# Optimization experiments

Measured on AMD Instinct MI355X. Metric: run time of the kernel, lower is better.

The kernel has to match this reference:

```python
import jax, jax.numpy as jnp
import numpy as np

N_NODES = 50000
N_EDGES = 800000
NFEAT, NHID, NCLASS = 512, 128, 16


def _with_self_loops(edge_idx, n):
    loop = jnp.arange(n, dtype=edge_idx.dtype)
    src = jnp.concatenate([edge_idx[0], loop])  # [E+N]
    dst = jnp.concatenate([edge_idx[1], loop])
    return src, dst


def gcn_conv(x, src, dst, W, b, n):
    # GCNConv with add aggregation, self-loops, symmetric normalization.
    h = x @ W  # [N, out]
    ones = jnp.ones(src.shape[0], dtype=h.dtype)
    deg = jax.ops.segment_sum(ones, dst, num_segments=n)  # in-degree incl. self-loops
    dinv = jnp.where(deg > 0, jax.lax.rsqrt(deg), 0.0)
    norm = dinv[src] * dinv[dst]  # [E+N]
    msg = h[src] * norm[:, None]  # gather + scale
    out = jax.ops.segment_sum(msg, dst, num_segments=n)  # scatter-add
    return out + b


def setup_inputs() -> dict:
    key = jax.random.key(0)
    ks = jax.random.split(key, 8)
    x = jax.random.normal(ks[0], (N_NODES, NFEAT), dtype=jnp.float32)
    edge_idx = jax.random.randint(ks[1], (2, N_EDGES), 0, N_NODES, dtype=jnp.int64)
    s1 = 1.0 / np.sqrt(NFEAT)
    s2 = 1.0 / np.sqrt(NHID)
    W1 = jax.random.uniform(ks[2], (NFEAT, NHID), jnp.float32, -s1, s1)
    b1 = jnp.zeros((NHID,), jnp.float32)
    W2 = jax.random.uniform(ks[3], (NHID, NHID), jnp.float32, -s2, s2)
    b2 = jnp.zeros((NHID,), jnp.float32)
    Wc = jax.random.uniform(ks[4], (NHID, NCLASS), jnp.float32, -s2, s2)
    bc = jax.random.uniform(ks[5], (NCLASS,), jnp.float32, -s2, s2)
    return {"x": x, "edge_idx": edge_idx, "W1": W1, "b1": b1, "W2": W2, "b2": b2, "Wc": Wc, "bc": bc}


def reference(x, edge_idx, W1, b1, W2, b2, Wc, bc):
    n = x.shape[0]
    src, dst = _with_self_loops(edge_idx, n)
    h = gcn_conv(x, src, dst, W1, b1, n)
    h = jax.nn.relu(h)  # dropout is identity in eval mode
    h = gcn_conv(h, src, dst, W2, b2, n)
    h = jax.nn.relu(h)
    logits = h @ Wc + bc
    return jax.nn.log_softmax(logits, axis=1)
```

## Files before the change

### kernel.cpp

```cpp
#include <hip/hip_runtime.h>
#include <math.h>

#define NFEAT 512
#define NHID  128
#define NCLASS 16
#define SCAN_BS 512
#define AGG_BLOCKS 1024
#define NSTREAMS 16384

typedef __attribute__((ext_vector_type(8))) short short8;
typedef __attribute__((ext_vector_type(4))) float f32x4;

static __device__ __forceinline__ ushort f2b(float f) {
    union { float f; uint u; } v; v.f = f;
    uint r = v.u + 0x7FFFu + ((v.u >> 16) & 1u);
    return (ushort)(r >> 16);
}
static __device__ __forceinline__ float b2f_lo(uint bits) {
    union { uint u; float f; } v; v.u = bits << 16; return v.f;
}
static __device__ __forceinline__ float b2f_hi(uint bits) {
    union { uint u; float f; } v; v.u = bits & 0xffff0000u; return v.f;
}


__global__ void k_init_tcast(const float* __restrict__ W1, const float* __restrict__ W2,
                             ushort* __restrict__ W1T, ushort* __restrict__ W2T,
                             int* __restrict__ deg, int n) {
    int idx = blockIdx.x * 256 + threadIdx.x;
    if (idx < n) deg[idx] = 1;
    if (idx < NFEAT * 128) {
        int k = idx >> 7, c = idx & 127;
        W1T[(size_t)c * NFEAT + k] = f2b(W1[idx]);
    } else {
        int j = idx - NFEAT * 128;
        if (j < NHID * 128) {
            int k = j >> 7, c = j & 127;
            W2T[(size_t)c * NHID + k] = f2b(W2[j]);
        }
    }
}

__global__ void k_count(const int* __restrict__ dst, int e, int* __restrict__ deg,
                        int* __restrict__ ticket) {
    int i = blockIdx.x * blockDim.x + threadIdx.x;
    if (i < e) ticket[i] = atomicAdd(&deg[dst[i]], 1);
}

__global__ void k_scan1(const int* __restrict__ deg, float* __restrict__ dinv,
                        int* __restrict__ offs, int* __restrict__ bsum, int n) {
    __shared__ int s[SCAN_BS];
    int t = threadIdx.x;
    int i = blockIdx.x * SCAN_BS + t;
    int d = (i < n) ? deg[i] : 0;
    if (i < n) dinv[i] = rsqrtf((float)d);
    s[t] = d;
    for (int off = 1; off < SCAN_BS; off <<= 1) {
        __syncthreads();
        int x = (t >= off) ? s[t - off] : 0;
        __syncthreads();
        s[t] += x;
    }
    __syncthreads();
    if (i < n) offs[i] = s[t] - d;
    if (t == SCAN_BS - 1) bsum[blockIdx.x] = s[t];
}

__global__ void k_scan3(int* __restrict__ offs, const int* __restrict__ bsum, int nb, int n) {
    __shared__ int pref[128];
    int t = threadIdx.x;
    if (t < 64) {
        int carry = 0;
        for (int base = 0; base < nb; base += 64) {
            int j = base + t;
            int v = (j < nb) ? bsum[j] : 0;
            for (int off = 1; off < 64; off <<= 1) {
                int x = __shfl_up(v, off);
                if (t >= off) v += x;
            }
            if (j < nb) pref[j] = carry + v;
            carry += __shfl(v, 63);
        }
    }
    __syncthreads();
    int i = blockIdx.x * SCAN_BS + t;
    int add = blockIdx.x ? pref[blockIdx.x - 1] : 0;
    if (i < n) offs[i] += add;
    if (blockIdx.x == 0 && t == 0) offs[n] = pref[nb - 1];
}

__global__ void k_fill_edges(const int* __restrict__ src, const int* __restrict__ dst, int e,
                             const int* __restrict__ eoffs, const int* __restrict__ ticket,
                             uint* __restrict__ colp32, int* __restrict__ rankgs,
                             int n, int S) {
    int i = blockIdx.x * blockDim.x + threadIdx.x;
    if (i < e) {
        colp32[eoffs[dst[i]] + ticket[i] - 1] = (uint)src[i];
    }
    if (i < n) {
        colp32[eoffs[i + 1] - 1] = (uint)i | ((uint)(i + 1) << 16);
    }
    if (i < NSTREAMS) {
        int len = (S + NSTREAMS - 1) / NSTREAMS;
        int target = i * len;
        int lo = 0, hi = n;
        while (lo < hi) {
            int mid = (lo + hi) >> 1;
            if (eoffs[mid] < target) lo = mid + 1; else hi = mid;
        }
        rankgs[i] = eoffs[lo];
        if (i == 0) rankgs[NSTREAMS] = S;
    }
    if (i == 0) {
#pragma unroll
        for (int k = 0; k < 8; k++) colp32[S + k] = 0;
    }
}


template<int A_F32>
__global__ __launch_bounds__(256) void k_gemm(const void* __restrict__ Aptr,
                                              const ushort* __restrict__ WT,
                                              const float* __restrict__ rowscale,
                                              ushort* __restrict__ Hs, int M, int K) {
    __shared__ ushort As[64][40];
    __shared__ ushort Bs[128][40];

    const int tid = threadIdx.x;
    const int wc = tid >> 6, lane = tid & 63;
    const int lr = lane & 15, lk = (lane >> 4) * 8;
    const int rowbase = blockIdx.x * 64;

    f32x4 acc[4][2];
#pragma unroll
    for (int i = 0; i < 4; i++)
#pragma unroll
        for (int j = 0; j < 2; j++) acc[i][j] = (f32x4)0.f;

    const int sr = tid >> 2;
    const int sh = (tid & 3) * 8;

    for (int k0 = 0; k0 < K; k0 += 32) {
        {
            int gr = rowbase + sr;
            ushort tmp[8];
            if (A_F32) {
                const float* A = (const float*)Aptr;
                if (gr < M) {
                    const float* p = A + (size_t)gr * K + k0 + sh;
#pragma unroll
                    for (int q = 0; q < 2; q++) {
                        float4 v = *(const float4*)(p + q * 4);
                        tmp[q * 4 + 0] = f2b(v.x); tmp[q * 4 + 1] = f2b(v.y);
                        tmp[q * 4 + 2] = f2b(v.z); tmp[q * 4 + 3] = f2b(v.w);
                    }
                } else {
#pragma unroll
                    for (int q = 0; q < 8; q++) tmp[q] = 0;
                }
            } else {
                const ushort* A = (const ushort*)Aptr;
                if (gr < M) {
                    *(short8*)&tmp[0] = *(const short8*)(A + (size_t)gr * K + k0 + sh);
                } else {
#pragma unroll
                    for (int q = 0; q < 8; q++) tmp[q] = 0;
                }
            }
            *(short8*)&As[sr][sh] = *(short8*)&tmp[0];
        }
        {
#pragma unroll
            for (int t = 0; t < 2; t++) {
                int c = tid + t * 256;
                int row = c >> 2, q = c & 3;
                short8 v = *(const short8*)(WT + (size_t)row * K + k0 + q * 8);
                *(short8*)&Bs[row][q * 8] = v;
            }
        }
        __syncthreads();

        short8 af[4], bfv[2];
#pragma unroll
        for (int i = 0; i < 4; i++) af[i] = *(const short8*)&As[i * 16 + lr][lk];
#pragma unroll
        for (int j = 0; j < 2; j++) bfv[j] = *(const short8*)&Bs[wc * 32 + j * 16 + lr][lk];
#pragma unroll
        for (int i = 0; i < 4; i++)
#pragma unroll
            for (int j = 0; j < 2; j++)
                acc[i][j] = __builtin_amdgcn_mfma_f32_16x16x32_bf16(af[i], bfv[j], acc[i][j], 0, 0, 0);
        __syncthreads();
    }

#pragma unroll
    for (int i = 0; i < 4; i++) {
#pragma unroll
        for (int r = 0; r < 4; r++) {
            int row = rowbase + i * 16 + (lane >> 4) * 4 + r;
            if (row < M) {
                float sc = rowscale[row];
#pragma unroll
                for (int j = 0; j < 2; j++) {
                    int f = j * 16 + lr;
                    Hs[((size_t)wc * M + row) * 32 + f] = f2b(acc[i][j][r] * sc);
                }
            }
        }
    }
}


__global__ __launch_bounds__(256) void k_aggs(const ushort* __restrict__ hs,
                                              const uint* __restrict__ colp32,
                                              const int* __restrict__ rankgs,
                                              const float* __restrict__ dinv,
                                              const float* __restrict__ bias,
                                              ushort* __restrict__ outp, int n) {
    const int b = blockIdx.x;
    const int s = b & 3;
    const int wid = threadIdx.x >> 6, lane = threadIdx.x & 63;
    const int st16 = lane >> 2, q = lane & 3;
    const int stream = (((b >> 2) << 2) + wid) * 16 + st16;
    int gs = rankgs[stream];
    int se = rankgs[stream + 1];
    bool alive = gs < se;
    int g = gs;

    const ushort* hsl = hs + (size_t)s * n * 32;
    const float4 bv0 = *(const float4*)(bias + s * 32 + q * 8);
    const float4 bv1 = *(const float4*)(bias + s * 32 + q * 8 + 4);

    const uint* cp = colp32 + g;
    uint cw0 = cp[0], cw1 = cp[1], cw2 = cp[2], cw3 = cp[3];
    uint4 pk0 = *(const uint4*)(hsl + (size_t)(cw0 & 0xffffu) * 32 + q * 8);
    uint4 pk1 = *(const uint4*)(hsl + (size_t)(cw1 & 0xffffu) * 32 + q * 8);
    uint4 pk2 = *(const uint4*)(hsl + (size_t)(cw2 & 0xffffu) * 32 + q * 8);
    float fdv0 = (cw0 >> 16) ? dinv[(cw0 >> 16) - 1] : 0.f;
    float fdv1 = (cw1 >> 16) ? dinv[(cw1 >> 16) - 1] : 0.f;
    float fdv2 = (cw2 >> 16) ? dinv[(cw2 >> 16) - 1] : 0.f;
    float a0 = 0.f, a1 = 0.f, a2 = 0.f, a3 = 0.f;
    float a4 = 0.f, a5 = 0.f, a6 = 0.f, a7 = 0.f;

    while (__any(alive)) {
        if (alive) {
            uint cw4 = cp[4];
            uint4 pk3 = *(const uint4*)(hsl + (size_t)(cw3 & 0xffffu) * 32 + q * 8);
            float fdv3 = (cw3 >> 16) ? dinv[(cw3 >> 16) - 1] : 0.f;

            a0 += b2f_lo(pk0.x); a1 += b2f_hi(pk0.x);
            a2 += b2f_lo(pk0.y); a3 += b2f_hi(pk0.y);
            a4 += b2f_lo(pk0.z); a5 += b2f_hi(pk0.z);
            a6 += b2f_lo(pk0.w); a7 += b2f_hi(pk0.w);

            if (cw0 >> 16) {
                int v = (int)(cw0 >> 16) - 1;
                float r0 = fmaxf(fmaf(a0, fdv0, bv0.x), 0.f);
                float r1 = fmaxf(fmaf(a1, fdv0, bv0.y), 0.f);
                float r2 = fmaxf(fmaf(a2, fdv0, bv0.z), 0.f);
                float r3 = fmaxf(fmaf(a3, fdv0, bv0.w), 0.f);
                float r4 = fmaxf(fmaf(a4, fdv0, bv1.x), 0.f);
                float r5 = fmaxf(fmaf(a5, fdv0, bv1.y), 0.f);
                float r6 = fmaxf(fmaf(a6, fdv0, bv1.z), 0.f);
                float r7 = fmaxf(fmaf(a7, fdv0, bv1.w), 0.f);
                uint4 u;
                u.x = (uint)f2b(r0) | ((uint)f2b(r1) << 16);
                u.y = (uint)f2b(r2) | ((uint)f2b(r3) << 16);
                u.z = (uint)f2b(r4) | ((uint)f2b(r5) << 16);
                u.w = (uint)f2b(r6) | ((uint)f2b(r7) << 16);
                *(uint4*)(outp + (size_t)v * 128 + s * 32 + q * 8) = u;
                a0 = a1 = a2 = a3 = a4 = a5 = a6 = a7 = 0.f;
                if (g + 1 >= se) alive = false;
            }
            g++; cp++;
            cw0 = cw1; cw1 = cw2; cw2 = cw3; cw3 = cw4;
            pk0 = pk1; pk1 = pk2; pk2 = pk3;
            fdv0 = fdv1; fdv1 = fdv2; fdv2 = fdv3;
        }
    }
}


__global__ __launch_bounds__(256) void k_classify(const ushort* __restrict__ h,
                                                  const float* __restrict__ Wc,
                                                  const float* __restrict__ bc,
                                                  float* __restrict__ out, int n) {
    __shared__ float Ws[128 * 16];
    int tid = threadIdx.x;
#pragma unroll
    for (int t = 0; t < 8; t++) Ws[tid + 256 * t] = Wc[tid + 256 * t];
    __syncthreads();

    int wid = tid >> 6, lane = tid & 63;
    int v = blockIdx.x * 4 + wid;
    if (v >= n) return;

    int j = lane & 15, c = lane >> 4;
    const ushort* hv = h + (size_t)v * 128 + c * 32;
    float acc = 0.f;
#pragma unroll
    for (int t = 0; t < 16; t++) {
        uint pk = *(const uint*)(hv + t * 2);
        acc = fmaf(b2f_lo(pk), Ws[(c * 32 + t * 2 + 0) * 16 + j], acc);
        acc = fmaf(b2f_hi(pk), Ws[(c * 32 + t * 2 + 1) * 16 + j], acc);
    }
    acc += __shfl_xor(acc, 16);
    acc += __shfl_xor(acc, 32);
    acc += bc[j];

    float m = acc;
#pragma unroll
    for (int o = 8; o >= 1; o >>= 1) m = fmaxf(m, __shfl_xor(m, o));
    float sum = expf(acc - m);
#pragma unroll
    for (int o = 8; o >= 1; o >>= 1) sum += __shfl_xor(sum, o);
    if (lane < 16) out[(size_t)v * 16 + j] = acc - m - logf(sum);
}


extern "C" void kernel_launch(void* const* d_in, const int* in_sizes, int n_in,
                              void* d_out, int out_size, void* d_ws, size_t ws_size,
                              hipStream_t stream) {
    const float* x  = (const float*)d_in[0];
    const int* eidx = (const int*)d_in[1];
    const float* W1 = (const float*)d_in[2];
    const float* b1 = (const float*)d_in[3];
    const float* W2 = (const float*)d_in[4];
    const float* b2 = (const float*)d_in[5];
    const float* Wc = (const float*)d_in[6];
    const float* bc = (const float*)d_in[7];
    float* out = (float*)d_out;

    const int N = in_sizes[0] / NFEAT;
    const int E = in_sizes[1] / 2;
    const int S = E + N;
    const int* src = eidx;
    const int* dst = eidx + E;

    char* p = (char*)d_ws;
    auto alloc = [&](size_t bytes) { char* r = p; p += (bytes + 255) & ~(size_t)255; return r; };
    int*    deg    = (int*)   alloc((size_t)N * 4);
    float*  dinv   = (float*) alloc((size_t)N * 4);
    int*    eoffs  = (int*)   alloc((size_t)(N + 1) * 4);
    int*    ticket = (int*)   alloc((size_t)E * 4);
    uint*   colp32 = (uint*)  alloc(((size_t)S + 16) * 4);
    int*    rankgs = (int*)   alloc((size_t)(NSTREAMS + 1) * 4);
    int*    bsum   = (int*)   alloc((size_t)256 * 4);
    ushort* W1T    = (ushort*)alloc((size_t)128 * NFEAT * 2);
    ushort* W2T    = (ushort*)alloc((size_t)128 * NHID * 2);
    ushort* hs     = (ushort*)alloc((size_t)N * NHID * 2);
    ushort* g1     = (ushort*)alloc((size_t)N * NHID * 2);
    ushort* g2     = (ushort*)alloc((size_t)N * NHID * 2);

    const int nb = (N + SCAN_BS - 1) / SCAN_BS;

    k_init_tcast<<<((NFEAT + NHID) * 128 + 255) / 256, 256, 0, stream>>>(W1, W2, W1T, W2T, deg, N);
    k_count<<<(E + 255) / 256, 256, 0, stream>>>(dst, E, deg, ticket);
    k_scan1<<<nb, SCAN_BS, 0, stream>>>(deg, dinv, eoffs, bsum, N);
    k_scan3<<<nb, SCAN_BS, 0, stream>>>(eoffs, bsum, nb, N);
    k_fill_edges<<<(E + 255) / 256, 256, 0, stream>>>(src, dst, E, eoffs, ticket, colp32,
                                                      rankgs, N, S);

    const int gblocks = (N + 63) / 64;
    k_gemm<1><<<gblocks, 256, 0, stream>>>(x, W1T, dinv, hs, N, NFEAT);
    k_aggs<<<AGG_BLOCKS, 256, 0, stream>>>(hs, colp32, rankgs, dinv, b1, g1, N);
    k_gemm<0><<<gblocks, 256, 0, stream>>>(g1, W2T, dinv, hs, N, NHID);
    k_aggs<<<AGG_BLOCKS, 256, 0, stream>>>(hs, colp32, rankgs, dinv, b2, g2, N);
    k_classify<<<(N + 3) / 4, 256, 0, stream>>>(g2, Wc, bc, out, N);
}
```

Baseline: 227.7 us.

## Fuse scan carry into edge fill and deepen aggregation gather prefetch

```diff
diff --git a/kernel.cpp b/kernel.cpp
--- a/kernel.cpp
+++ b/kernel.cpp
@@ -66,39 +66,39 @@
     if (t == SCAN_BS - 1) bsum[blockIdx.x] = s[t];
 }
 
-__global__ void k_scan3(int* __restrict__ offs, const int* __restrict__ bsum, int nb, int n) {
-    __shared__ int pref[128];
-    int t = threadIdx.x;
-    if (t < 64) {
+__global__ void k_fill_edges(const int* __restrict__ src, const int* __restrict__ dst, int e,
+                             const int* __restrict__ offs, const int* __restrict__ bsum,
+                             const int* __restrict__ ticket, uint* __restrict__ colp32,
+                             int* __restrict__ rankgs, int n, int S, int nbch) {
+    __shared__ int incl[128];
+    int tid = threadIdx.x;
+    if (tid < 64) {
         int carry = 0;
-        for (int base = 0; base < nb; base += 64) {
-            int j = base + t;
-            int v = (j < nb) ? bsum[j] : 0;
+        for (int base = 0; base < nbch; base += 64) {
+            int j = base + tid;
+            int v = (j < nbch) ? bsum[j] : 0;
             for (int off = 1; off < 64; off <<= 1) {
                 int x = __shfl_up(v, off);
-                if (t >= off) v += x;
-            }
-            if (j < nb) pref[j] = carry + v;
+                if (tid >= off) v += x;
+            }
+            if (j < nbch) incl[j] = carry + v;
             carry += __shfl(v, 63);
         }
     }
     __syncthreads();
-    int i = blockIdx.x * SCAN_BS + t;
-    int add = blockIdx.x ? pref[blockIdx.x - 1] : 0;
-    if (i < n) offs[i] += add;
-    if (blockIdx.x == 0 && t == 0) offs[n] = pref[nb - 1];
-}
-
-__global__ void k_fill_edges(const int* __restrict__ src, const int* __restrict__ dst, int e,
-                             const int* __restrict__ eoffs, const int* __restrict__ ticket,
-                             uint* __restrict__ colp32, int* __restrict__ rankgs,
-                             int n, int S) {
-    int i = blockIdx.x * blockDim.x + threadIdx.x;
+
+    auto absoff = [&](int v) -> int {
+        if (v >= n) return S;
+        int c = v >> 9;
+        return offs[v] + (c ? incl[c - 1] : 0);
+    };
+
+    int i = blockIdx.x * blockDim.x + tid;
     if (i < e) {
-        colp32[eoffs[dst[i]] + ticket[i] - 1] = (uint)src[i];
+        colp32[absoff(dst[i]) + ticket[i] - 1] = (uint)src[i];
     }
     if (i < n) {
-        colp32[eoffs[i + 1] - 1] = (uint)i | ((uint)(i + 1) << 16);
+        colp32[absoff(i + 1) - 1] = (uint)i | ((uint)(i + 1) << 16);
     }
     if (i < NSTREAMS) {
         int len = (S + NSTREAMS - 1) / NSTREAMS;
@@ -106,9 +106,9 @@
         int lo = 0, hi = n;
         while (lo < hi) {
             int mid = (lo + hi) >> 1;
-            if (eoffs[mid] < target) lo = mid + 1; else hi = mid;
-        }
-        rankgs[i] = eoffs[lo];
+            if (absoff(mid) < target) lo = mid + 1; else hi = mid;
+        }
+        rankgs[i] = absoff(lo);
         if (i == 0) rankgs[NSTREAMS] = S;
     }
     if (i == 0) {
@@ -222,31 +222,33 @@
     const int wid = threadIdx.x >> 6, lane = threadIdx.x & 63;
     const int st16 = lane >> 2, q = lane & 3;
     const int stream = (((b >> 2) << 2) + wid) * 16 + st16;
-    int gs = rankgs[stream];
+    int g = rankgs[stream];
     int se = rankgs[stream + 1];
-    bool alive = gs < se;
-    int g = gs;
+    bool alive = g < se;
+    if (!alive) g = 0;
 
     const ushort* hsl = hs + (size_t)s * n * 32;
     const float4 bv0 = *(const float4*)(bias + s * 32 + q * 8);
     const float4 bv1 = *(const float4*)(bias + s * 32 + q * 8 + 4);
 
     const uint* cp = colp32 + g;
-    uint cw0 = cp[0], cw1 = cp[1], cw2 = cp[2], cw3 = cp[3];
+    uint cw0 = cp[0], cw1 = cp[1], cw2 = cp[2], cw3 = cp[3], cw4 = cp[4];
     uint4 pk0 = *(const uint4*)(hsl + (size_t)(cw0 & 0xffffu) * 32 + q * 8);
     uint4 pk1 = *(const uint4*)(hsl + (size_t)(cw1 & 0xffffu) * 32 + q * 8);
     uint4 pk2 = *(const uint4*)(hsl + (size_t)(cw2 & 0xffffu) * 32 + q * 8);
+    uint4 pk3 = *(const uint4*)(hsl + (size_t)(cw3 & 0xffffu) * 32 + q * 8);
     float fdv0 = (cw0 >> 16) ? dinv[(cw0 >> 16) - 1] : 0.f;
     float fdv1 = (cw1 >> 16) ? dinv[(cw1 >> 16) - 1] : 0.f;
     float fdv2 = (cw2 >> 16) ? dinv[(cw2 >> 16) - 1] : 0.f;
+    float fdv3 = (cw3 >> 16) ? dinv[(cw3 >> 16) - 1] : 0.f;
     float a0 = 0.f, a1 = 0.f, a2 = 0.f, a3 = 0.f;
     float a4 = 0.f, a5 = 0.f, a6 = 0.f, a7 = 0.f;
 
     while (__any(alive)) {
         if (alive) {
-            uint cw4 = cp[4];
-            uint4 pk3 = *(const uint4*)(hsl + (size_t)(cw3 & 0xffffu) * 32 + q * 8);
-            float fdv3 = (cw3 >> 16) ? dinv[(cw3 >> 16) - 1] : 0.f;
+            uint cw5 = cp[5];
+            uint4 pk4 = *(const uint4*)(hsl + (size_t)(cw4 & 0xffffu) * 32 + q * 8);
+            float fdv4 = (cw4 >> 16) ? dinv[(cw4 >> 16) - 1] : 0.f;
 
             a0 += b2f_lo(pk0.x); a1 += b2f_hi(pk0.x);
             a2 += b2f_lo(pk0.y); a3 += b2f_hi(pk0.y);
@@ -273,9 +275,9 @@
                 if (g + 1 >= se) alive = false;
             }
             g++; cp++;
-            cw0 = cw1; cw1 = cw2; cw2 = cw3; cw3 = cw4;
-            pk0 = pk1; pk1 = pk2; pk2 = pk3;
-            fdv0 = fdv1; fdv1 = fdv2; fdv2 = fdv3;
+            cw0 = cw1; cw1 = cw2; cw2 = cw3; cw3 = cw4; cw4 = cw5;
+            pk0 = pk1; pk1 = pk2; pk2 = pk3; pk3 = pk4;
+            fdv0 = fdv1; fdv1 = fdv2; fdv2 = fdv3; fdv3 = fdv4;
         }
     }
 }
@@ -357,9 +359,8 @@
     k_init_tcast<<<((NFEAT + NHID) * 128 + 255) / 256, 256, 0, stream>>>(W1, W2, W1T, W2T, deg, N);
     k_count<<<(E + 255) / 256, 256, 0, stream>>>(dst, E, deg, ticket);
     k_scan1<<<nb, SCAN_BS, 0, stream>>>(deg, dinv, eoffs, bsum, N);
-    k_scan3<<<nb, SCAN_BS, 0, stream>>>(eoffs, bsum, nb, N);
-    k_fill_edges<<<(E + 255) / 256, 256, 0, stream>>>(src, dst, E, eoffs, ticket, colp32,
-                                                      rankgs, N, S);
+    k_fill_edges<<<(E + 255) / 256, 256, 0, stream>>>(src, dst, E, eoffs, bsum, ticket,
+                                                      colp32, rankgs, N, S, nb);
 
     const int gblocks = (N + 63) / 64;
     k_gemm<1><<<gblocks, 256, 0, stream>>>(x, W1T, dinv, hs, N, NFEAT);
```

Result: no change. 228.8 us (+0.5%).
